# Kernel optimization log

Hardware: AMD Instinct MI355X
Metric: run time of the kernel (lower is better)

Reference implementation:

```python
import jax, jax.numpy as jnp
import numpy as np

HIDDEN = 64

def setup_inputs() -> dict:
    key = jax.random.key(0)
    ks = jax.random.split(key, 5)
    N, T, D, H = 4096, 128, 32, HIDDEN
    x = jax.random.normal(ks[0], (N, T, D), dtype=jnp.float32)
    adj_matrix = jax.random.uniform(ks[1], (N, N), dtype=jnp.float32) * (1.0 / N)
    weight_ih = jax.random.normal(ks[2], (D, 4 * H), dtype=jnp.float32) * (1.0 / np.sqrt(D))
    weight_hh = jax.random.normal(ks[3], (H, 4 * H), dtype=jnp.float32) * (1.0 / np.sqrt(H))
    bias = jnp.zeros((4 * H,), dtype=jnp.float32)
    weight_q = jax.random.normal(ks[4], (H, H), dtype=jnp.float32) * (1.0 / np.sqrt(H))
    bias_q = jnp.zeros((H,), dtype=jnp.float32)
    return {"x": x, "adj_matrix": adj_matrix, "weight_ih": weight_ih,
            "weight_hh": weight_hh, "bias": bias, "weight_q": weight_q,
            "bias_q": bias_q}

def reference(x, adj_matrix, weight_ih, weight_hh, bias, weight_q, bias_q):
    # x: [N, T, D]; adj_matrix: [N, N]. Dropout=0 -> identity (eval mode).
    N, T, D = x.shape
    H = weight_hh.shape[0]

    def step(carry, x_t):
        h, c = carry                                   # [N, H], [N, H]
        gates = x_t @ weight_ih + h @ weight_hh + bias  # [N, 4H]
        i_t = jax.nn.sigmoid(gates[:, :H])
        f_t = jax.nn.sigmoid(gates[:, H:2 * H])
        g_t = jnp.tanh(gates[:, 2 * H:3 * H])
        o_t = jax.nn.sigmoid(gates[:, 3 * H:])
        q_t = jnp.tanh(h @ weight_q + bias_q)           # [N, H]
        c_new = f_t * (c + adj_matrix @ q_t) + i_t * g_t
        h_new = o_t * jnp.tanh(c_new)
        return (h_new, c_new), h_new

    h0 = jnp.zeros((N, H), dtype=x.dtype)
    c0 = jnp.zeros((N, H), dtype=x.dtype)
    xs = jnp.swapaxes(x, 0, 1)                          # [T, N, D]
    _, hs = jax.lax.scan(step, (h0, c0), xs)            # hs: [T, N, H]
    return jnp.swapaxes(hs, 0, 1)                       # [N, T, H]
```

## Files before the change

kernel.cpp:

```cpp
#include <hip/hip_runtime.h>

typedef __attribute__((ext_vector_type(8))) short short8;
typedef __attribute__((ext_vector_type(4))) float f32x4;
typedef __attribute__((ext_vector_type(2))) float f32x2;
typedef __attribute__((ext_vector_type(2))) unsigned short us2;
typedef __attribute__((ext_vector_type(2))) long lx2;

#define N_NODES 4096
#define T_STEPS 128
#define H_DIM   64
#define NBLK    256
#define NTHR    512
#define ROWS    16

#define WS_FLAGS 0u
#define WS_WT    32768u
#define WS_WQT   81920u
#define WS_SYNC  90112u
#define WS_Q0    98304u
#define WS_Q1    360448u
#define WS_LFLAG 622592u
#define WS_NEED  1146880u

#define ADJ_STRIDE_B 4112u
#define ADJ_BYTES  (16u * ADJ_STRIDE_B)
#define GATE_BYTES 16384u
#define S_BYTES    4224u
#define C_BYTES    4096u
#define H_BYTES    2304u
#define SMEM_TOT   (ADJ_BYTES + GATE_BYTES + S_BYTES + C_BYTES + H_BYTES)

__device__ __forceinline__ unsigned short f2bf(float f) {
    unsigned x = __float_as_uint(f);
    unsigned r = ((x >> 16) & 1u) + 0x7fffu;
    return (unsigned short)((x + r) >> 16);
}
__device__ __forceinline__ short8 cvt8_trunc_v(f32x4 a, f32x4 b) {
    union { unsigned u[4]; short8 s; } cv;
    cv.u[0] = __builtin_amdgcn_perm(__float_as_uint(a[1]), __float_as_uint(a[0]), 0x07060302u);
    cv.u[1] = __builtin_amdgcn_perm(__float_as_uint(a[3]), __float_as_uint(a[2]), 0x07060302u);
    cv.u[2] = __builtin_amdgcn_perm(__float_as_uint(b[1]), __float_as_uint(b[0]), 0x07060302u);
    cv.u[3] = __builtin_amdgcn_perm(__float_as_uint(b[3]), __float_as_uint(b[2]), 0x07060302u);
    return cv.s;
}
__device__ __forceinline__ float fast_sigmoid(float x) { return 1.f / (1.f + __expf(-x)); }
__device__ __forceinline__ float fast_tanh(float x)    { return 1.f - 2.f / (1.f + __expf(2.f * x)); }

__device__ __forceinline__ void grid_barrier(int* flags, int bid, int tid, int epoch) {
    __syncthreads();
    if (tid == 0) {
        __builtin_amdgcn_fence(__ATOMIC_RELEASE, "agent");
        __hip_atomic_store(&flags[bid * 32], epoch, __ATOMIC_RELAXED, __HIP_MEMORY_SCOPE_AGENT);
    }
    if (tid < NBLK) {
        int guard = 0;
        while (__hip_atomic_load(&flags[tid * 32], __ATOMIC_RELAXED, __HIP_MEMORY_SCOPE_AGENT) < epoch) {
            __builtin_amdgcn_s_sleep(32);
            if (++guard > (1 << 17)) break;
        }
    }
    __syncthreads();
    if (tid == 0) __builtin_amdgcn_fence(__ATOMIC_ACQUIRE, "agent");
    __syncthreads();
}

#define MFMA16(a, b, c)  __builtin_amdgcn_mfma_f32_16x16x32_bf16((a), (b), (c), 0, 0, 0)
#define MFMAF8(a, b, c)  __builtin_amdgcn_mfma_f32_16x16x32_fp8_fp8((a), (b), (c), 0, 0, 0)

#define QLD4(dst, ptr, off) \
    asm volatile("global_load_dwordx4 %0, %1, off offset:" #off " sc0 sc1" \
                 : "=v"(dst) : "v"(ptr))
#define ISSUE_ST(dst, pp) do { \
    QLD4((dst)[0], (pp), 0);    QLD4((dst)[1], (pp), 1024); \
    QLD4((dst)[2], (pp), 2048); QLD4((dst)[3], (pp), 3072); \
} while (0)
#define WAITV(n) do { asm volatile("s_waitcnt vmcnt(" #n ")" ::: "memory"); \
                      __builtin_amdgcn_sched_barrier(0); } while (0)

__global__ __launch_bounds__(NTHR, 1) void glstm_kernel(
    const float* __restrict__ x,
    const float* __restrict__ adj,
    const float* __restrict__ w_ih,
    const float* __restrict__ w_hh,
    const float* __restrict__ bias,
    const float* __restrict__ w_q,
    const float* __restrict__ bias_q,
    float* __restrict__ out,
    unsigned char* __restrict__ ws)
{
    const int tid  = threadIdx.x;
    const int bid  = blockIdx.x;
    const int wave = tid >> 6;
    const int lane = tid & 63;
    const int l15  = lane & 15;
    const int quad = lane >> 4;
    const int rowbase = bid * ROWS;

    int* flags  = (int*)(ws + WS_FLAGS);
    int* lflags = (int*)(ws + WS_LFLAG);
    unsigned short* Wt  = (unsigned short*)(ws + WS_WT);
    unsigned short* Wqt = (unsigned short*)(ws + WS_WQT);
    unsigned char* qb0 = ws + WS_Q0;
    unsigned char* qb1 = ws + WS_Q1;

    extern __shared__ unsigned char smem[];
    unsigned char* adj_lds = smem;
    float* gate_lds = (float*)(smem + ADJ_BYTES);
    float* s_lds    = (float*)(smem + ADJ_BYTES + GATE_BYTES);
    float* c_lds    = (float*)(smem + ADJ_BYTES + GATE_BYTES + S_BYTES);
    unsigned short* h_lds = (unsigned short*)(smem + ADJ_BYTES + GATE_BYTES + S_BYTES + C_BYTES);

    if (tid < 96) {
        float v = (tid < 32) ? w_ih[tid * 256 + bid] : w_hh[(tid - 32) * 256 + bid];
        Wt[bid * 96 + tid] = f2bf(v);
    }
    if (bid < 64 && tid < 64) Wqt[bid * 64 + tid] = f2bf(w_q[tid * 64 + bid]);
    if (tid == 0) lflags[bid * 32] = 0;
    for (int idx = tid; idx < ROWS * 64; idx += NTHR) {
        int r = idx >> 6, hh = idx & 63;
        int n = rowbase + r, no = n & 63;
        float v = fast_tanh(bias_q[hh]);
        qb0[(size_t)(n >> 6) * 4096 + (hh >> 4) * 1024 + (hh & 15) * 64
            + ((no >> 3) & 3) * 16 + (no >> 5) * 8 + (no & 7)]
            = (unsigned char)(__builtin_amdgcn_cvt_pk_fp8_f32(v, v, 0, false) & 0xFF);
    }
    for (int idx = tid; idx < ROWS * 64; idx += NTHR) {
        int r = idx >> 6, cc = idx & 63;
        c_lds[r * 64 + cc] = 0.f;
        s_lds[r * 66 + cc] = 0.f;
        h_lds[r * 72 + cc] = 0;
    }
    for (int idx = tid; idx < ROWS * (N_NODES / 2); idx += NTHR) {
        int r = idx >> 11, c2 = idx & (N_NODES / 2 - 1);
        f32x2 av = *(const f32x2*)(adj + (size_t)(rowbase + r) * N_NODES + c2 * 2);
        int pk = __builtin_amdgcn_cvt_pk_fp8_f32(av[0] * 4096.f, av[1] * 4096.f, 0, false);
        *(unsigned short*)(adj_lds + r * ADJ_STRIDE_B + c2 * 2) = (unsigned short)pk;
    }
    grid_barrier(flags, bid, tid, 1);

    const int g    = wave >> 1;
    const int half = wave & 1;
    const int nc0  = g * 64 + half * 32 + l15;
    short8 wA[2][3];
#pragma unroll
    for (int nt = 0; nt < 2; ++nt)
#pragma unroll
        for (int kk = 0; kk < 3; ++kk)
            wA[nt][kk] = *(const short8*)(Wt + (nc0 + nt * 16) * 96 + kk * 32 + quad * 8);
    const float bv0 = bias[nc0], bv1 = bias[nc0 + 16];
    const int hhq = (wave & 3) * 16 + l15;
    short8 wQ[2];
#pragma unroll
    for (int kk = 0; kk < 2; ++kk)
        wQ[kk] = *(const short8*)(Wqt + hhq * 64 + kk * 32 + quad * 8);
    const float bqv = bias_q[hhq];

    const float* xlane = x + (size_t)(rowbase + l15) * T_STEPS * 32 + quad * 8;
    const unsigned char* albase = adj_lds + l15 * ADJ_STRIDE_B + wave * 512 + quad * 8;
    const int no0 = ((bid & 3) << 4) + (quad << 2);
    const size_t qdoff = (size_t)(bid >> 2) * 4096 + (size_t)(wave & 3) * 1024
                       + (size_t)l15 * 64 + ((no0 >> 3) & 3) * 16 + (no0 >> 5) * 8 + (no0 & 7);
    const int prodb = (wave << 5) + (lane & 31);

    f32x4 xa = *(const f32x4*)(xlane);
    f32x4 xb = *(const f32x4*)(xlane + 4);

    auto phaseA = [&]() {
        f32x4 acc0 = {0.f, 0.f, 0.f, 0.f};
        f32x4 acc1 = {0.f, 0.f, 0.f, 0.f};
        short8 a0 = cvt8_trunc_v(xa, xb);
        acc0 = MFMA16(a0, wA[0][0], acc0);
        acc1 = MFMA16(a0, wA[1][0], acc1);
#pragma unroll
        for (int kk = 1; kk < 3; ++kk) {
            short8 a = *(const short8*)(h_lds + l15 * 72 + (kk - 1) * 32 + quad * 8);
            acc0 = MFMA16(a, wA[0][kk], acc0);
            acc1 = MFMA16(a, wA[1][kk], acc1);
        }
#pragma unroll
        for (int nt = 0; nt < 2; ++nt) {
            f32x4 acc = nt ? acc1 : acc0;
            float bv  = nt ? bv1 : bv0;
            int colg  = half * 32 + nt * 16 + l15;
#pragma unroll
            for (int r = 0; r < 4; ++r) {
                float v = acc[r] + bv;
                v = (g == 2) ? fast_tanh(v) : fast_sigmoid(v);
                gate_lds[(g * 16 + quad * 4 + r) * 64 + colg] = v;
            }
        }
    };

    phaseA();
    xa = *(const f32x4*)(xlane + 32);
    xb = *(const f32x4*)(xlane + 36);

    const int rot = bid & 7;

    for (int t = 0; t < T_STEPS; ++t) {
        const unsigned char* qcur = (t & 1) ? qb1 : qb0;
        unsigned char*       qnxt = (t & 1) ? qb0 : qb1;

        {
            if (lane < 32) {
                int guard = 0;
                while (__hip_atomic_load(&lflags[prodb * 32],
                                         __ATOMIC_RELAXED, __HIP_MEMORY_SCOPE_AGENT) < t) {
                    __builtin_amdgcn_s_sleep(4);
                    if (++guard > (1 << 17)) break;
                }
            }
            f32x4 acc[4];
#pragma unroll
            for (int nt = 0; nt < 4; ++nt) acc[nt] = (f32x4){0.f, 0.f, 0.f, 0.f};
            const unsigned char* qp = qcur + ((size_t)wave << 15) + (l15 << 6) + (quad << 4);
            lx2 buf[3][4];
            ISSUE_ST(buf[0], qp + (size_t)(((0 + rot) & 7)) * 4096);
            ISSUE_ST(buf[1], qp + (size_t)(((1 + rot) & 7)) * 4096);
#pragma unroll
            for (int gg = 0; gg < 8; ++gg) {
                const int s = (gg + rot) & 7;
                if (gg < 6) {
                    const int s2 = (gg + 2 + rot) & 7;
                    ISSUE_ST(buf[(gg + 2) % 3], qp + (size_t)s2 * 4096);
                }
                long a0_ = *(const long*)(albase + s * 64);
                long a1_ = *(const long*)(albase + s * 64 + 32);
                if (gg < 6)       WAITV(8);
                else if (gg == 6) WAITV(4);
                else              WAITV(0);
                acc[0] = MFMAF8(a0_, buf[gg % 3][0][0], acc[0]);
                acc[1] = MFMAF8(a0_, buf[gg % 3][1][0], acc[1]);
                acc[2] = MFMAF8(a0_, buf[gg % 3][2][0], acc[2]);
                acc[3] = MFMAF8(a0_, buf[gg % 3][3][0], acc[3]);
                acc[0] = MFMAF8(a1_, buf[gg % 3][0][1], acc[0]);
                acc[1] = MFMAF8(a1_, buf[gg % 3][1][1], acc[1]);
                acc[2] = MFMAF8(a1_, buf[gg % 3][2][1], acc[2]);
                acc[3] = MFMAF8(a1_, buf[gg % 3][3][1], acc[3]);
            }
#pragma unroll
            for (int nt = 0; nt < 4; ++nt)
#pragma unroll
                for (int r = 0; r < 4; ++r)
                    atomicAdd(&s_lds[(quad * 4 + r) * 66 + nt * 16 + l15],
                              acc[nt][r] * (1.0f / 4096.0f));
        }
        __syncthreads();

        {
            const int r  = tid >> 5;
            const int c0 = (tid & 31) * 2;
            float hn[2];
#pragma unroll
            for (int j = 0; j < 2; ++j) {
                int cc = c0 + j;
                float s = s_lds[r * 66 + cc];
                s_lds[r * 66 + cc] = 0.f;
                float iv = gate_lds[(0 * 16 + r) * 64 + cc];
                float fv = gate_lds[(1 * 16 + r) * 64 + cc];
                float gv = gate_lds[(2 * 16 + r) * 64 + cc];
                float ov = gate_lds[(3 * 16 + r) * 64 + cc];
                float cn = fv * (c_lds[r * 64 + cc] + s) + iv * gv;
                hn[j] = ov * fast_tanh(cn);
                c_lds[r * 64 + cc] = cn;
            }
            us2 hv; hv[0] = f2bf(hn[0]); hv[1] = f2bf(hn[1]);
            *(us2*)(h_lds + r * 72 + c0) = hv;
            *(f32x2*)(out + ((size_t)(rowbase + r) * T_STEPS + t) * H_DIM + c0) = (f32x2){hn[0], hn[1]};
        }
        __syncthreads();

        if (t < T_STEPS - 1) {
            if (wave < 4) {
                f32x4 acc = {0.f, 0.f, 0.f, 0.f};
#pragma unroll
                for (int kk = 0; kk < 2; ++kk) {
                    short8 a = *(const short8*)(h_lds + l15 * 72 + kk * 32 + quad * 8);
                    acc = MFMA16(a, wQ[kk], acc);
                }
                float q0 = fast_tanh(acc[0] + bqv), q1 = fast_tanh(acc[1] + bqv);
                float q2 = fast_tanh(acc[2] + bqv), q3 = fast_tanh(acc[3] + bqv);
                int pk = __builtin_amdgcn_cvt_pk_fp8_f32(q0, q1, 0, false);
                pk     = __builtin_amdgcn_cvt_pk_fp8_f32(q2, q3, pk, true);
                unsigned char* qdst = qnxt + qdoff;
                asm volatile("global_store_dword %0, %1, off sc0 sc1" :: "v"(qdst), "v"(pk) : "memory");
            }
            phaseA();
            if (t < T_STEPS - 2) {
                xa = *(const f32x4*)(xlane + (t + 2) * 32);
                xb = *(const f32x4*)(xlane + (t + 2) * 32 + 4);
            }
            asm volatile("s_waitcnt vmcnt(0)" ::: "memory");
            __syncthreads();
            if (tid == 0)
                __hip_atomic_store(&lflags[bid * 32], t + 1,
                                   __ATOMIC_RELAXED, __HIP_MEMORY_SCOPE_AGENT);
        }
    }
}

extern "C" void kernel_launch(void* const* d_in, const int* in_sizes, int n_in,
                              void* d_out, int out_size, void* d_ws, size_t ws_size,
                              hipStream_t stream) {
    if (ws_size < WS_NEED) return;
    const float* x      = (const float*)d_in[0];
    const float* adj    = (const float*)d_in[1];
    const float* w_ih   = (const float*)d_in[2];
    const float* w_hh   = (const float*)d_in[3];
    const float* bias   = (const float*)d_in[4];
    const float* w_q    = (const float*)d_in[5];
    const float* bias_q = (const float*)d_in[6];
    float* o = (float*)d_out;
    unsigned char* w = (unsigned char*)d_ws;

    hipFuncSetAttribute((const void*)glstm_kernel,
                        hipFuncAttributeMaxDynamicSharedMemorySize, SMEM_TOT);
    glstm_kernel<<<NBLK, NTHR, SMEM_TOT, stream>>>(x, adj, w_ih, w_hh, bias, w_q, bias_q, o, w);
}
```

Baseline: 2.351 ms.

## Publish step flag before phase A and issue all q loads up front

Moves the per-block flag store ahead of the phaseA gate computation and the x prefetch, so consumer blocks waiting on this block's q can proceed sooner while phaseA overlaps their wait. The adjacency-times-q loop drops its 3-deep rotating buffer and issues all 8 q slices at once, draining with decreasing vmcnt waits. The spin-wait sleep is doubled. This raises register pressure (32 outstanding 16-byte loads per lane), and the added vmcnt(0) before the loop makes it wait on the x prefetch too.

```diff
diff --git a/kernel.cpp b/kernel.cpp
--- a/kernel.cpp
+++ b/kernel.cpp
@@ -16,7 +16,6 @@
 #define WS_FLAGS 0u
 #define WS_WT    32768u
 #define WS_WQT   81920u
-#define WS_SYNC  90112u
 #define WS_Q0    98304u
 #define WS_Q1    360448u
 #define WS_LFLAG 622592u
@@ -76,6 +75,20 @@
 } while (0)
 #define WAITV(n) do { asm volatile("s_waitcnt vmcnt(" #n ")" ::: "memory"); \
                       __builtin_amdgcn_sched_barrier(0); } while (0)
+#define BSTEP(gg, W) do { \
+    const int s_ = ((gg) + rot) & 7; \
+    long a0_ = *(const long*)(albase + s_ * 64);         \
+    long a1_ = *(const long*)(albase + s_ * 64 + 32);    \
+    WAITV(W); \
+    acc[0] = MFMAF8(a0_, buf[gg][0][0], acc[0]); \
+    acc[1] = MFMAF8(a0_, buf[gg][1][0], acc[1]); \
+    acc[2] = MFMAF8(a0_, buf[gg][2][0], acc[2]); \
+    acc[3] = MFMAF8(a0_, buf[gg][3][0], acc[3]); \
+    acc[0] = MFMAF8(a1_, buf[gg][0][1], acc[0]); \
+    acc[1] = MFMAF8(a1_, buf[gg][1][1], acc[1]); \
+    acc[2] = MFMAF8(a1_, buf[gg][2][1], acc[2]); \
+    acc[3] = MFMAF8(a1_, buf[gg][3][1], acc[3]); \
+} while (0)
 
 __global__ __launch_bounds__(NTHR, 1) void glstm_kernel(
     const float* __restrict__ x,
@@ -206,38 +219,21 @@
                 int guard = 0;
                 while (__hip_atomic_load(&lflags[prodb * 32],
                                          __ATOMIC_RELAXED, __HIP_MEMORY_SCOPE_AGENT) < t) {
-                    __builtin_amdgcn_s_sleep(4);
+                    __builtin_amdgcn_s_sleep(8);
                     if (++guard > (1 << 17)) break;
                 }
             }
+            WAITV(0);
             f32x4 acc[4];
 #pragma unroll
             for (int nt = 0; nt < 4; ++nt) acc[nt] = (f32x4){0.f, 0.f, 0.f, 0.f};
             const unsigned char* qp = qcur + ((size_t)wave << 15) + (l15 << 6) + (quad << 4);
-            lx2 buf[3][4];
-            ISSUE_ST(buf[0], qp + (size_t)(((0 + rot) & 7)) * 4096);
-            ISSUE_ST(buf[1], qp + (size_t)(((1 + rot) & 7)) * 4096);
-#pragma unroll
-            for (int gg = 0; gg < 8; ++gg) {
-                const int s = (gg + rot) & 7;
-                if (gg < 6) {
-                    const int s2 = (gg + 2 + rot) & 7;
-                    ISSUE_ST(buf[(gg + 2) % 3], qp + (size_t)s2 * 4096);
-                }
-                long a0_ = *(const long*)(albase + s * 64);
-                long a1_ = *(const long*)(albase + s * 64 + 32);
-                if (gg < 6)       WAITV(8);
-                else if (gg == 6) WAITV(4);
-                else              WAITV(0);
-                acc[0] = MFMAF8(a0_, buf[gg % 3][0][0], acc[0]);
-                acc[1] = MFMAF8(a0_, buf[gg % 3][1][0], acc[1]);
-                acc[2] = MFMAF8(a0_, buf[gg % 3][2][0], acc[2]);
-                acc[3] = MFMAF8(a0_, buf[gg % 3][3][0], acc[3]);
-                acc[0] = MFMAF8(a1_, buf[gg % 3][0][1], acc[0]);
-                acc[1] = MFMAF8(a1_, buf[gg % 3][1][1], acc[1]);
-                acc[2] = MFMAF8(a1_, buf[gg % 3][2][1], acc[2]);
-                acc[3] = MFMAF8(a1_, buf[gg % 3][3][1], acc[3]);
-            }
+            lx2 buf[8][4];
+#pragma unroll
+            for (int ii = 0; ii < 8; ++ii)
+                ISSUE_ST(buf[ii], qp + (size_t)((ii + rot) & 7) * 4096);
+            BSTEP(0, 28); BSTEP(1, 24); BSTEP(2, 20); BSTEP(3, 16);
+            BSTEP(4, 12); BSTEP(5, 8);  BSTEP(6, 4);  BSTEP(7, 0);
 #pragma unroll
             for (int nt = 0; nt < 4; ++nt)
 #pragma unroll
@@ -285,16 +281,16 @@
                 unsigned char* qdst = qnxt + qdoff;
                 asm volatile("global_store_dword %0, %1, off sc0 sc1" :: "v"(qdst), "v"(pk) : "memory");
             }
-            phaseA();
-            if (t < T_STEPS - 2) {
-                xa = *(const f32x4*)(xlane + (t + 2) * 32);
-                xb = *(const f32x4*)(xlane + (t + 2) * 32 + 4);
-            }
             asm volatile("s_waitcnt vmcnt(0)" ::: "memory");
             __syncthreads();
             if (tid == 0)
                 __hip_atomic_store(&lflags[bid * 32], t + 1,
                                    __ATOMIC_RELAXED, __HIP_MEMORY_SCOPE_AGENT);
+            phaseA();
+            if (t < T_STEPS - 2) {
+                xa = *(const f32x4*)(xlane + (t + 2) * 32);
+                xb = *(const f32x4*)(xlane + (t + 2) * 32 + 4);
+            }
         }
     }
 }
```

Measured after the change: 2.128 ms. 9.5% less time.
